# Optimization experiments

Measured on AMD Instinct MI355X. Metric: run time of the kernel, lower is better.

Reference implementation:

```python
import jax, jax.numpy as jnp
import numpy as np

TAU = 0.1          # contrastive_temperature
EPS = 0.05         # property_epsilon
L_LOCAL_G, L_GLOBAL, L_SC_G, L_LOCAL_SC, G_PROP = 1.0, 0.8, 1.0, 0.8, 0.5
B = 4096
D = 256
NUM_PROPS = 4
N_ATOMS = 131072
N_MOTIFS = 32768


def setup_inputs() -> dict:
    key = jax.random.key(0)
    ks = jax.random.split(key, 10)
    return {
        "emb_g_mole": jax.random.normal(ks[0], (B, D), jnp.float32),
        "emb_g_frag": jax.random.normal(ks[1], (N_ATOMS, D), jnp.float32),
        "emb_sc_mole": jax.random.normal(ks[2], (B, D), jnp.float32),
        "emb_sc_shape": jax.random.normal(ks[3], (N_MOTIFS, D), jnp.float32),
        "emb_motif": jax.random.normal(ks[4], (N_MOTIFS, D), jnp.float32),
        "emb_shape": jax.random.normal(ks[5], (N_MOTIFS, D), jnp.float32),
        # scaled so duplicate rows are the only pairs within EPS (realistic sparse mask)
        "prop_pred": jax.random.normal(ks[6], (B, NUM_PROPS), jnp.float32) * 0.05,
        "prop_target": jax.random.normal(ks[7], (B, NUM_PROPS), jnp.float32) * 0.05,
        "batch_g": jax.random.randint(ks[8], (N_ATOMS,), 0, B, jnp.int32),
        "batch_sc": jax.random.randint(ks[9], (N_MOTIFS,), 0, B, jnp.int32),
    }


def _contrastive(emb, props):
    # SupervisedContrastiveLoss: normalized cosine logits, mask from sqrt(cdist) < eps
    n = emb.shape[0]
    e = emb / jnp.maximum(jnp.linalg.norm(emb, axis=1, keepdims=True), 1e-12)
    logits = jnp.matmul(e, e.T) / TAU                       # [n, n]
    log_probs = jax.nn.log_softmax(logits, axis=1)
    sq = jnp.sum(props * props, axis=1)
    d2 = jnp.maximum(sq[:, None] + sq[None, :] - 2.0 * jnp.matmul(props, props.T), 0.0)
    dd = jnp.sqrt(jnp.sqrt(d2)) + 1e-8                      # cdist(...).sqrt() + 1e-8
    mask = (dd < EPS) & (~jnp.eye(n, dtype=bool))           # fill_diagonal_(0)
    cnt = jnp.sum(mask, axis=1)
    row_loss = -jnp.sum(jnp.where(mask, log_probs, 0.0), axis=1) / jnp.maximum(cnt, 1)
    valid = cnt > 0
    nvalid = jnp.sum(valid)
    loss = jnp.sum(jnp.where(valid, row_loss, 0.0)) / jnp.maximum(nvalid, 1)
    return jnp.where(nvalid > 0, loss, 0.0)


def _frag_alignment(emb_g_frag, emb_motif, batch_g, batch_sc):
    ones_g = jnp.ones((emb_g_frag.shape[0],), emb_g_frag.dtype)
    ones_s = jnp.ones((emb_motif.shape[0],), emb_motif.dtype)
    cnt_g = jax.ops.segment_sum(ones_g, batch_g, num_segments=B)
    cnt_s = jax.ops.segment_sum(ones_s, batch_sc, num_segments=B)
    mean_g = jax.ops.segment_sum(emb_g_frag, batch_g, num_segments=B) / jnp.maximum(cnt_g, 1.0)[:, None]
    mean_s = jax.ops.segment_sum(emb_motif, batch_sc, num_segments=B) / jnp.maximum(cnt_s, 1.0)[:, None]
    norms = jnp.linalg.norm(mean_g - mean_s, axis=1)
    valid = (cnt_g > 0) & (cnt_s > 0)
    batch_size = batch_g.max().astype(emb_g_frag.dtype) + 1.0
    return jnp.sum(jnp.where(valid, norms, 0.0)) / batch_size


def reference(emb_g_mole, emb_g_frag, emb_sc_mole, emb_sc_shape, emb_motif,
              emb_shape, prop_pred, prop_target, batch_g, batch_sc):
    l_local_g = _frag_alignment(emb_g_frag, emb_motif, batch_g, batch_sc)
    combined_emb = jnp.concatenate([emb_g_mole, emb_sc_mole], axis=0)    # [2B, d]
    combined_props = jnp.concatenate([prop_pred, prop_pred], axis=0)      # [2B, p]
    l_contr = _contrastive(combined_emb, combined_props)
    l_global = l_contr          # same inputs in both calls -> identical value
    l_local_sc = l_contr
    l_sc_g = jnp.mean(jnp.linalg.norm(emb_sc_shape - emb_shape, axis=1))  # AlignmentLoss mean
    l_prop = jnp.mean((prop_pred - prop_target) ** 2)                     # MSELoss
    l_hes = (L_LOCAL_G * l_local_g + L_GLOBAL * l_global + L_SC_G * l_sc_g
             + L_LOCAL_SC * l_local_sc + G_PROP * l_prop)
    # stacked: [l_hes, l_local_g, l_global, l_sc_g, l_local_sc, l_prop]
    return jnp.stack([l_hes, l_local_g, l_global, l_sc_g, l_local_sc, l_prop])
```

## Files before the change

kernel.cpp:

```cpp
#include <hip/hip_runtime.h>
#include <hip/hip_bf16.h>
#include <stdint.h>

typedef unsigned short u16;
typedef float f32x4 __attribute__((ext_vector_type(4)));
typedef short s16x8 __attribute__((ext_vector_type(8)));
typedef u16   u16x8 __attribute__((ext_vector_type(8)));
typedef u16   u16x4 __attribute__((ext_vector_type(4)));
typedef uint32_t u32x4 __attribute__((ext_vector_type(4)));

#define B_      4096
#define D_      256
#define NA_     131072
#define NM_     32768
#define N2_     8192
#define THR4    6.2499950e-6f
#define K2E     14.426950408889634f
#define CAPG    96
#define CAPS    40

#define NS_   1024
#define NG_   2080
#define NT_   256
#define NTOT_ 3360
#define NR_   2336

#define OFF_CNT_G   0u
#define OFF_CNT_S   16384u
#define OFF_NB      32768u
#define OFF_SCAL    49152u
#define OFF_S       65536u
#define ZERO_BYTES  98304u
#define OFF_T       98304u
#define OFF_C       131072u
#define OFF_PLIST   163840u
#define OFF_LIST_G  688128u
#define OFF_LIST_S  2260992u
#define OFF_E       2916352u
#define WS_NEED     7110656u

__device__ inline float wave_sum(float v) {
#pragma unroll
  for (int m = 1; m < 64; m <<= 1) v += __shfl_xor(v, m, 64);
  return v;
}
__device__ inline int wave_sum_i(int v) {
#pragma unroll
  for (int m = 1; m < 64; m <<= 1) v += __shfl_xor(v, m, 64);
  return v;
}
__device__ inline u16 f2bf(float f) {
  uint32_t u = __float_as_uint(f);
  uint32_t r = (u + 0x7FFFu + ((u >> 16) & 1u)) >> 16;
  return (u16)r;
}
__device__ inline float bf2f(u16 v) { return __uint_as_float(((uint32_t)v) << 16); }

__device__ inline f32x4 ldnt4(const float* p) {
  return __builtin_nontemporal_load((const f32x4*)p);
}

__device__ inline void gload16(const u16* __restrict__ g, u16* l) {
  __builtin_amdgcn_global_load_lds(
      (const __attribute__((address_space(1))) uint32_t*)g,
      (__attribute__((address_space(3))) uint32_t*)l, 16, 0, 0);
}

__global__ void k_zero(u32x4* __restrict__ p) {
  u32x4 z = {0u, 0u, 0u, 0u};
  p[blockIdx.x * 256 + threadIdx.x] = z;
}

__global__ __launch_bounds__(256) void k_fuseA(
    const int* __restrict__ bg, const int* __restrict__ bs,
    int* __restrict__ cntg, int* __restrict__ cnts, int* __restrict__ bmax,
    int* __restrict__ listg, int* __restrict__ lists,
    const float* __restrict__ gm, const float* __restrict__ scm,
    const float* __restrict__ scs, const float* __restrict__ shp,
    const float* __restrict__ pp,
    u16* __restrict__ E, int* __restrict__ nb, int* __restrict__ plist,
    float* __restrict__ scal) {
  int t = threadIdx.x, w = t >> 6, lane = t & 63;
  int blk = blockIdx.x;

  if (blk < 512) {
    int i = blk * 256 + t;
    int b = -1;
    if (i < NA_) {
      b = bg[i];
      int pos = atomicAdd(&cntg[b], 1);
      if (pos < CAPG) listg[b * CAPG + pos] = i;
    }
    if (i < NM_) {
      int b2 = bs[i];
      int pos = atomicAdd(&cnts[b2], 1);
      if (pos < CAPS) lists[b2 * CAPS + pos] = i;
    }
    int m = b;
#pragma unroll
    for (int k = 1; k < 64; k <<= 1) m = max(m, __shfl_xor(m, k, 64));
    if ((t & 63) == 0 && m >= 0) atomicMax(bmax, m);
  } else if (blk < 4608) {
    int a = blk - 512;
    f32x4 pa = *(const f32x4*)(pp + (size_t)a * 4);
    for (int b = t; b < B_; b += 256) {
      f32x4 pb = *(const f32x4*)(pp + (size_t)b * 4);
      float dx = pa.x - pb.x, dy = pa.y - pb.y, dz = pa.z - pb.z, dw = pa.w - pb.w;
      float d2 = dx * dx + dy * dy + dz * dz + dw * dw;
      if (d2 < THR4) {
        int pos = atomicAdd(&nb[a], 1);
        if (pos < 32) plist[a * 32 + pos] = b;
      }
    }
  } else if (blk < 6656) {
    int r = (blk - 4608) * 4 + w;
    const float* src = (r < B_) ? gm + (size_t)r * D_ : scm + (size_t)(r - B_) * D_;
    f32x4 v = ldnt4(src + lane * 4);
    float ss = v.x * v.x + v.y * v.y + v.z * v.z + v.w * v.w;
    ss = wave_sum(ss);
    float inv = 1.f / fmaxf(sqrtf(ss), 1e-12f);
    u16x4 o;
    o.x = f2bf(v.x * inv); o.y = f2bf(v.y * inv);
    o.z = f2bf(v.z * inv); o.w = f2bf(v.w * inv);
    *(u16x4*)(E + (size_t)r * D_ + lane * 4) = o;
  } else {
    int wg = (blk - 6656) * 4 + w;
    float acc = 0.f;
    for (int r = wg; r < NM_; r += 8192) {
      f32x4 va = ldnt4(scs + (size_t)r * D_ + lane * 4);
      f32x4 vb = ldnt4(shp + (size_t)r * D_ + lane * 4);
      float dx = va.x - vb.x, dy = va.y - vb.y, dz = va.z - vb.z, dw = va.w - vb.w;
      float ss = wave_sum(dx * dx + dy * dy + dz * dz + dw * dw);
      if (lane == 0) acc += sqrtf(ss);
    }
    __shared__ float sr4[4];
    if (lane == 0) sr4[w] = acc;
    __syncthreads();
    if (t == 0) atomicAdd(&scal[1], sr4[0] + sr4[1] + sr4[2] + sr4[3]);
  }
}

__device__ inline void wave_row_sum(const float* __restrict__ src,
                                    const int* __restrict__ list,
                                    int off, int cnt, int lane, f32x4* accs) {
  f32x4 a0 = {0.f,0.f,0.f,0.f}, a1 = a0, a2 = a0, a3 = a0;
  f32x4 a4 = a0, a5 = a0, a6 = a0, a7 = a0;
  for (int base = 0; base < cnt; base += 64) {
    int n = min(cnt - base, 64);
    int idx = (lane < n) ? list[off + base + lane] : 0;
    int k = 0;
    for (; k + 7 < n; k += 8) {
      int i0 = __shfl(idx, k,     64), i1 = __shfl(idx, k + 1, 64);
      int i2 = __shfl(idx, k + 2, 64), i3 = __shfl(idx, k + 3, 64);
      int i4 = __shfl(idx, k + 4, 64), i5 = __shfl(idx, k + 5, 64);
      int i6 = __shfl(idx, k + 6, 64), i7 = __shfl(idx, k + 7, 64);
      a0 += ldnt4(src + (size_t)i0 * D_ + lane * 4);
      a1 += ldnt4(src + (size_t)i1 * D_ + lane * 4);
      a2 += ldnt4(src + (size_t)i2 * D_ + lane * 4);
      a3 += ldnt4(src + (size_t)i3 * D_ + lane * 4);
      a4 += ldnt4(src + (size_t)i4 * D_ + lane * 4);
      a5 += ldnt4(src + (size_t)i5 * D_ + lane * 4);
      a6 += ldnt4(src + (size_t)i6 * D_ + lane * 4);
      a7 += ldnt4(src + (size_t)i7 * D_ + lane * 4);
    }
    for (; k < n; k++) {
      int i0 = __shfl(idx, k, 64);
      a0 += ldnt4(src + (size_t)i0 * D_ + lane * 4);
    }
  }
  *accs = ((a0 + a1) + (a2 + a3)) + ((a4 + a5) + (a6 + a7));
}

__global__ __launch_bounds__(256) void k_fuseB(
    const u16* __restrict__ E,
    const float* __restrict__ fg, const float* __restrict__ fm,
    const int* __restrict__ cntg, const int* __restrict__ cnts,
    const int* __restrict__ listg, const int* __restrict__ lists,
    const int* __restrict__ nb, const int* __restrict__ plist,
    float* __restrict__ S, float* __restrict__ T, int* __restrict__ C,
    float* __restrict__ scal) {
  __shared__ __align__(16) u16 As[128 * 64];
  __shared__ __align__(16) u16 Bs[128 * 64];
  int blk = blockIdx.x;
  int tid = threadIdx.x, lane = tid & 63, wid = tid >> 6;

  int64_t p = (int64_t)blk * NS_;
  int srem = (int)(p % NTOT_);
  if (srem < NS_) {
    int sid = (int)(p / NTOT_);
    int b = sid * 4 + wid;
    int cg = cntg[b], cs = cnts[b];
    f32x4 sg, ss;
    wave_row_sum(fg, listg, b * CAPG, min(cg, CAPG), lane, &sg);
    wave_row_sum(fm, lists, b * CAPS, min(cs, CAPS), lane, &ss);
    float ig = 1.f / fmaxf((float)cg, 1.f);
    float is = 1.f / fmaxf((float)cs, 1.f);
    float dx = sg.x * ig - ss.x * is, dy = sg.y * ig - ss.y * is;
    float dz = sg.z * ig - ss.z * is, dw = sg.w * ig - ss.w * is;
    float v = wave_sum(dx * dx + dy * dy + dz * dz + dw * dw);
    __shared__ float r2[4];
    if (lane == 0) r2[wid] = (cg > 0 && cs > 0) ? sqrtf(v) : 0.f;
    __syncthreads();
    if (tid == 0) {
      float s = r2[0] + r2[1] + r2[2] + r2[3];
      if (s != 0.f) atomicAdd(&scal[0], s);
    }
    return;
  }

  int r = blk - (int)((p + NTOT_ - 1) / NTOT_);
  int64_t q = (int64_t)r * NG_;
  int grem = (int)(q % NR_);

  if (grem >= NG_) {
    int tix = r - (int)((q + NR_ - 1) / NR_);
#pragma unroll
    for (int k8 = 0; k8 < 8; k8++) {
      int i = tix * 32 + wid * 8 + k8;
      int a = i & (B_ - 1);
      int n = min(nb[a], 32);
      u16x4 vi = *(const u16x4*)(E + (size_t)i * D_ + lane * 4);
      float ex = bf2f(vi.x), ey = bf2f(vi.y), ez = bf2f(vi.z), ew = bf2f(vi.w);
      float acc = -(ex * ex + ey * ey + ez * ez + ew * ew);
      for (int k = 0; k < n; k++) {
        int b = plist[a * 32 + k];
        u16x4 v1 = *(const u16x4*)(E + (size_t)b * D_ + lane * 4);
        u16x4 v2 = *(const u16x4*)(E + (size_t)(b + B_) * D_ + lane * 4);
        acc += ex * bf2f(v1.x) + ey * bf2f(v1.y) + ez * bf2f(v1.z) + ew * bf2f(v1.w);
        acc += ex * bf2f(v2.x) + ey * bf2f(v2.y) + ez * bf2f(v2.z) + ew * bf2f(v2.w);
      }
      acc = wave_sum(acc);
      if (lane == 0) { T[i] = 10.0f * acc; C[i] = 2 * n - 1; }
    }
    return;
  }

  int t = (int)(q / NR_);
  int bi = (int)((129.0f - sqrtf(129.0f * 129.0f - 8.0f * (float)t)) * 0.5f);
  while ((bi + 1) * (129 - (bi + 1)) / 2 <= t) bi++;
  while (bi * (129 - bi) / 2 > t) bi--;
  int bj = bi + (t - bi * (129 - bi) / 2);

  int row0 = bi * 128, col0 = bj * 128;
  int wr = wid >> 1, wc = wid & 1;

  int rsub = lane >> 3;
  int csw  = (((lane & 7) ^ rsub) << 4) >> 1;

  f32x4 acc[4][4];
#pragma unroll
  for (int mi = 0; mi < 4; mi++)
#pragma unroll
    for (int ni = 0; ni < 4; ni++) {
      f32x4 z = {0.f, 0.f, 0.f, 0.f};
      acc[mi][ni] = z;
    }

  for (int kc = 0; kc < 4; ++kc) {
    __syncthreads();
#pragma unroll
    for (int it = 0; it < 4; it++) {
      int s = wid * 4 + it;
      int rr = s * 8 + rsub;
      gload16(E + (size_t)(row0 + rr) * D_ + kc * 64 + csw, As + s * 512);
      gload16(E + (size_t)(col0 + rr) * D_ + kc * 64 + csw, Bs + s * 512);
    }
    __syncthreads();
#pragma unroll
    for (int kk = 0; kk < 2; ++kk) {
      s16x8 af[4], bfr[4];
#pragma unroll
      for (int mi = 0; mi < 4; mi++) {
        int rA = wr * 64 + mi * 16 + (lane & 15);
        int cbf = kk * 64 + (lane >> 4) * 16;
        int addr = rA * 128 + (cbf ^ ((rA & 7) << 4));
        af[mi] = *(const s16x8*)((const char*)As + addr);
      }
#pragma unroll
      for (int ni = 0; ni < 4; ni++) {
        int rB = wc * 64 + ni * 16 + (lane & 15);
        int cbf = kk * 64 + (lane >> 4) * 16;
        int addr = rB * 128 + (cbf ^ ((rB & 7) << 4));
        bfr[ni] = *(const s16x8*)((const char*)Bs + addr);
      }
#pragma unroll
      for (int mi = 0; mi < 4; mi++)
#pragma unroll
        for (int ni = 0; ni < 4; ni++)
          acc[mi][ni] = __builtin_amdgcn_mfma_f32_16x16x32_bf16(af[mi], bfr[ni], acc[mi][ni], 0, 0, 0);
    }
  }

  int g = lane >> 4, cl = lane & 15;
  float colsum[4] = {0.f, 0.f, 0.f, 0.f};
#pragma unroll
  for (int mi = 0; mi < 4; mi++) {
#pragma unroll
    for (int reg = 0; reg < 4; ++reg) {
      int gi = row0 + wr * 64 + mi * 16 + g * 4 + reg;
      float vs = 0.f;
#pragma unroll
      for (int ni = 0; ni < 4; ni++) {
        float e = exp2f(acc[mi][ni][reg] * K2E - K2E);
        vs += e;
        colsum[ni] += e;
      }
#pragma unroll
      for (int m = 1; m < 16; m <<= 1) vs += __shfl_xor(vs, m, 64);
      if (cl == 0) atomicAdd(&S[gi], vs);
    }
  }
  if (bi != bj) {
#pragma unroll
    for (int ni = 0; ni < 4; ni++) {
      float cs = colsum[ni];
      cs += __shfl_xor(cs, 16, 64);
      cs += __shfl_xor(cs, 32, 64);
      if (g == 0) atomicAdd(&S[col0 + wc * 64 + ni * 16 + cl], cs);
    }
  }
}

__global__ void k_final(const float* __restrict__ S, const float* __restrict__ T,
                        const int* __restrict__ C, const float* __restrict__ scal,
                        const float* __restrict__ pp, const float* __restrict__ pt,
                        float* __restrict__ out) {
  float sp = 0.f;
  for (int i = threadIdx.x; i < B_ * 4; i += 256) {
    float d = pp[i] - pt[i];
    sp += d * d;
  }
  float rls = 0.f; int nv = 0;
  for (int i = threadIdx.x; i < N2_; i += 256) {
    int ci = C[i];
    if (ci > 0) { rls += (10.0f + logf(S[i])) - T[i] / (float)ci; nv++; }
  }
  rls = wave_sum(rls);
  sp  = wave_sum(sp);
  nv  = wave_sum_i(nv);
  __shared__ float r1[4], r3[4]; __shared__ int r2[4];
  int lane = threadIdx.x & 63, w = threadIdx.x >> 6;
  if (lane == 0) { r1[w] = rls; r2[w] = nv; r3[w] = sp; }
  __syncthreads();
  if (threadIdx.x == 0) {
    float rtot = r1[0] + r1[1] + r1[2] + r1[3];
    int nvt = r2[0] + r2[1] + r2[2] + r2[3];
    float sptot = r3[0] + r3[1] + r3[2] + r3[3];
    float l_contr = nvt > 0 ? rtot / (float)nvt : 0.f;
    int bmax = ((const int*)scal)[3];
    float bs = (float)bmax + 1.0f;
    float l_local_g = scal[0] / bs;
    float l_sc = scal[1] / (float)NM_;
    float l_prop = sptot / (float)(B_ * 4);
    float l_hes = 1.0f * l_local_g + 0.8f * l_contr + 1.0f * l_sc + 0.8f * l_contr + 0.5f * l_prop;
    out[0] = l_hes; out[1] = l_local_g; out[2] = l_contr;
    out[3] = l_sc;  out[4] = l_contr;   out[5] = l_prop;
  }
}

extern "C" void kernel_launch(void* const* d_in, const int* in_sizes, int n_in,
                              void* d_out, int out_size, void* d_ws, size_t ws_size,
                              hipStream_t stream) {
  if (ws_size < WS_NEED) return;
  const float* gm  = (const float*)d_in[0];
  const float* fg  = (const float*)d_in[1];
  const float* scm = (const float*)d_in[2];
  const float* scs = (const float*)d_in[3];
  const float* mot = (const float*)d_in[4];
  const float* shp = (const float*)d_in[5];
  const float* pp  = (const float*)d_in[6];
  const float* pt  = (const float*)d_in[7];
  const int* bg = (const int*)d_in[8];
  const int* bs = (const int*)d_in[9];
  float* out = (float*)d_out;
  char* ws = (char*)d_ws;

  int* cntg  = (int*)(ws + OFF_CNT_G);
  int* cnts  = (int*)(ws + OFF_CNT_S);
  int* nb    = (int*)(ws + OFF_NB);
  float* scal = (float*)(ws + OFF_SCAL);
  float* S   = (float*)(ws + OFF_S);
  float* T   = (float*)(ws + OFF_T);
  int* C     = (int*)(ws + OFF_C);
  int* plist = (int*)(ws + OFF_PLIST);
  int* listg = (int*)(ws + OFF_LIST_G);
  int* lists = (int*)(ws + OFF_LIST_S);
  u16* E     = (u16*)(ws + OFF_E);

  k_zero<<<24, 256, 0, stream>>>((u32x4*)ws);
  k_fuseA<<<8704, 256, 0, stream>>>(bg, bs, cntg, cnts, (int*)scal + 3,
                                    listg, lists, gm, scm, scs, shp, pp,
                                    E, nb, plist, scal);
  k_fuseB<<<NTOT_, 256, 0, stream>>>(E, fg, mot, cntg, cnts, listg, lists,
                                     nb, plist, S, T, C, scal);
  k_final<<<1, 256, 0, stream>>>(S, T, C, scal, pp, pt, out);
}
```

Measured before the change: 202.8 us.

## Interleave fuseA block roles, halve GEMM K-chunk LDS tiles, use fast log2

```diff
diff --git a/kernel.cpp b/kernel.cpp
--- a/kernel.cpp
+++ b/kernel.cpp
@@ -16,6 +16,7 @@
 #define N2_     8192
 #define THR4    6.2499950e-6f
 #define K2E     14.426950408889634f
+#define LN2_    0.6931471805599453f
 #define CAPG    96
 #define CAPS    40
 
@@ -57,7 +58,7 @@
 __device__ inline float bf2f(u16 v) { return __uint_as_float(((uint32_t)v) << 16); }
 
 __device__ inline f32x4 ldnt4(const float* p) {
-  return __builtin_nontemporal_load((const f32x4*)p);
+  return __builtin_nontemporal_load((const f32x4*)(p));
 }
 
 __device__ inline void gload16(const u16* __restrict__ g, u16* l) {
@@ -83,8 +84,9 @@
   int t = threadIdx.x, w = t >> 6, lane = t & 63;
   int blk = blockIdx.x;
 
-  if (blk < 512) {
-    int i = blk * 256 + t;
+  if (blk % 17 == 0) {
+    int aid = blk / 17;
+    int i = aid * 256 + t;
     int b = -1;
     if (i < NA_) {
       b = bg[i];
@@ -100,8 +102,12 @@
 #pragma unroll
     for (int k = 1; k < 64; k <<= 1) m = max(m, __shfl_xor(m, k, 64));
     if ((t & 63) == 0 && m >= 0) atomicMax(bmax, m);
-  } else if (blk < 4608) {
-    int a = blk - 512;
+    return;
+  }
+  int r1 = blk - blk / 17 - 1;
+
+  if (!(r1 & 1)) {
+    int a = r1 >> 1;
     f32x4 pa = *(const f32x4*)(pp + (size_t)a * 4);
     for (int b = t; b < B_; b += 256) {
       f32x4 pb = *(const f32x4*)(pp + (size_t)b * 4);
@@ -112,8 +118,12 @@
         if (pos < 32) plist[a * 32 + pos] = b;
       }
     }
-  } else if (blk < 6656) {
-    int r = (blk - 4608) * 4 + w;
+    return;
+  }
+  int r3 = r1 >> 1;
+
+  if (!(r3 & 1)) {
+    int r = (r3 >> 1) * 4 + w;
     const float* src = (r < B_) ? gm + (size_t)r * D_ : scm + (size_t)(r - B_) * D_;
     f32x4 v = ldnt4(src + lane * 4);
     float ss = v.x * v.x + v.y * v.y + v.z * v.z + v.w * v.w;
@@ -124,7 +134,7 @@
     o.z = f2bf(v.z * inv); o.w = f2bf(v.w * inv);
     *(u16x4*)(E + (size_t)r * D_ + lane * 4) = o;
   } else {
-    int wg = (blk - 6656) * 4 + w;
+    int wg = (r3 >> 1) * 4 + w;
     float acc = 0.f;
     for (int r = wg; r < NM_; r += 8192) {
       f32x4 va = ldnt4(scs + (size_t)r * D_ + lane * 4);
@@ -179,8 +189,8 @@
     const int* __restrict__ nb, const int* __restrict__ plist,
     float* __restrict__ S, float* __restrict__ T, int* __restrict__ C,
     float* __restrict__ scal) {
-  __shared__ __align__(16) u16 As[128 * 64];
-  __shared__ __align__(16) u16 Bs[128 * 64];
+  __shared__ __align__(16) u16 As[128 * 32];
+  __shared__ __align__(16) u16 Bs[128 * 32];
   int blk = blockIdx.x;
   int tid = threadIdx.x, lane = tid & 63, wid = tid >> 6;
 
@@ -244,8 +254,8 @@
   int row0 = bi * 128, col0 = bj * 128;
   int wr = wid >> 1, wc = wid & 1;
 
-  int rsub = lane >> 3;
-  int csw  = (((lane & 7) ^ rsub) << 4) >> 1;
+  int rsub = lane >> 2;
+  int csw  = (((lane & 3) ^ (rsub & 3)) << 3);
 
   f32x4 acc[4][4];
 #pragma unroll
@@ -256,39 +266,34 @@
       acc[mi][ni] = z;
     }
 
-  for (int kc = 0; kc < 4; ++kc) {
+  for (int kc = 0; kc < 8; ++kc) {
     __syncthreads();
 #pragma unroll
-    for (int it = 0; it < 4; it++) {
-      int s = wid * 4 + it;
-      int rr = s * 8 + rsub;
-      gload16(E + (size_t)(row0 + rr) * D_ + kc * 64 + csw, As + s * 512);
-      gload16(E + (size_t)(col0 + rr) * D_ + kc * 64 + csw, Bs + s * 512);
+    for (int it = 0; it < 2; it++) {
+      int s = wid * 2 + it;
+      int rr = s * 16 + rsub;
+      gload16(E + (size_t)(row0 + rr) * D_ + kc * 32 + csw, As + s * 512);
+      gload16(E + (size_t)(col0 + rr) * D_ + kc * 32 + csw, Bs + s * 512);
     }
     __syncthreads();
-#pragma unroll
-    for (int kk = 0; kk < 2; ++kk) {
-      s16x8 af[4], bfr[4];
-#pragma unroll
-      for (int mi = 0; mi < 4; mi++) {
-        int rA = wr * 64 + mi * 16 + (lane & 15);
-        int cbf = kk * 64 + (lane >> 4) * 16;
-        int addr = rA * 128 + (cbf ^ ((rA & 7) << 4));
-        af[mi] = *(const s16x8*)((const char*)As + addr);
-      }
-#pragma unroll
-      for (int ni = 0; ni < 4; ni++) {
-        int rB = wc * 64 + ni * 16 + (lane & 15);
-        int cbf = kk * 64 + (lane >> 4) * 16;
-        int addr = rB * 128 + (cbf ^ ((rB & 7) << 4));
-        bfr[ni] = *(const s16x8*)((const char*)Bs + addr);
-      }
-#pragma unroll
-      for (int mi = 0; mi < 4; mi++)
-#pragma unroll
-        for (int ni = 0; ni < 4; ni++)
-          acc[mi][ni] = __builtin_amdgcn_mfma_f32_16x16x32_bf16(af[mi], bfr[ni], acc[mi][ni], 0, 0, 0);
-    }
+    s16x8 af[4], bfr[4];
+#pragma unroll
+    for (int mi = 0; mi < 4; mi++) {
+      int rA = wr * 64 + mi * 16 + (lane & 15);
+      int addr = rA * 64 + (((lane >> 4) * 16) ^ ((rA & 3) << 4));
+      af[mi] = *(const s16x8*)((const char*)As + addr);
+    }
+#pragma unroll
+    for (int ni = 0; ni < 4; ni++) {
+      int rB = wc * 64 + ni * 16 + (lane & 15);
+      int addr = rB * 64 + (((lane >> 4) * 16) ^ ((rB & 3) << 4));
+      bfr[ni] = *(const s16x8*)((const char*)Bs + addr);
+    }
+#pragma unroll
+    for (int mi = 0; mi < 4; mi++)
+#pragma unroll
+      for (int ni = 0; ni < 4; ni++)
+        acc[mi][ni] = __builtin_amdgcn_mfma_f32_16x16x32_bf16(af[mi], bfr[ni], acc[mi][ni], 0, 0, 0);
   }
 
   int g = lane >> 4, cl = lane & 15;
@@ -333,7 +338,7 @@
   float rls = 0.f; int nv = 0;
   for (int i = threadIdx.x; i < N2_; i += 256) {
     int ci = C[i];
-    if (ci > 0) { rls += (10.0f + logf(S[i])) - T[i] / (float)ci; nv++; }
+    if (ci > 0) { rls += (10.0f + __log2f(S[i]) * LN2_) - T[i] / (float)ci; nv++; }
   }
   rls = wave_sum(rls);
   sp  = wave_sum(sp);
```

Result: no change. 200.1 us (median of 2 runs) (-1.3%).
